# Kernel tuning notes

Hardware: AMD Instinct MI355X
Metric: run time of the kernel (lower is better)

## Reference

```python
import jax, jax.numpy as jnp
import numpy as np

BETA = 0.25
N_E = 1024
E_DIM = 64


def setup_inputs() -> dict:
    key = jax.random.key(0)
    k1, k2 = jax.random.split(key)
    z = jax.random.normal(k1, (32, E_DIM, 64, 64), dtype=jnp.float32)  # (B,C,H,W)
    emb = jax.random.uniform(k2, (N_E, E_DIM), dtype=jnp.float32,
                             minval=-1.0 / N_E, maxval=1.0 / N_E)
    return {"z": z, "embedding": emb}


def reference(z, embedding):
    # (B,C,H,W) -> (B,H,W,C)
    z_nhwc = jnp.transpose(z, (0, 2, 3, 1))
    zf = z_nhwc.reshape(-1, E_DIM)  # (N, C)
    # squared L2 distances: ||z||^2 + ||e||^2 - 2 z e^T  -> (N, n_e)
    d = (jnp.sum(zf * zf, axis=1, keepdims=True)
         + jnp.sum(embedding * embedding, axis=1)
         - 2.0 * jnp.matmul(zf, embedding.T))
    min_encoding_indices = jnp.argmin(d, axis=1)[:, None]  # (N,1)
    idx = min_encoding_indices[:, 0]
    min_encodings = jax.nn.one_hot(idx, N_E, dtype=jnp.float32)  # (N, n_e)
    # codebook lookup (equivalent to one-hot matmul)
    z_q = embedding[idx].reshape(z_nhwc.shape)  # (B,H,W,C)
    loss = (jnp.mean((jax.lax.stop_gradient(z_q) - z_nhwc) ** 2)
            + BETA * jnp.mean((z_q - jax.lax.stop_gradient(z_nhwc)) ** 2))
    # straight-through estimator
    z_q = z_nhwc + jax.lax.stop_gradient(z_q - z_nhwc)
    e_mean = jnp.mean(min_encodings, axis=0)
    perplexity = jnp.exp(-jnp.sum(e_mean * jnp.log(e_mean + 1e-10)))
    z_q = jnp.transpose(z_q, (0, 3, 1, 2))  # (B,C,H,W)
    return (loss, z_q, perplexity, min_encodings, min_encoding_indices)
```

## Files before the change

### kernel.cpp

```cpp
#include <hip/hip_runtime.h>

#define N_PIX   (32 * 64 * 64)
#define E_DIM   64
#define N_E     1024
#define Z_ELEMS (N_PIX * E_DIM)

#define LOSS_OFF 0
#define ZQ_OFF   1
#define PERP_OFF (1 + Z_ELEMS)
#define ENC_OFF  ((size_t)(2 + Z_ELEMS))
#define IDX_OFF  (ENC_OFF + (size_t)N_PIX * N_E)

#define WS_COUNTS   0
#define WS_LOSS     4096
#define WS_EE       8192
#define WS_EMB16    12288
#define WS_MINV     143360
#define WS_KEYS     667648
#define WS_CAND     1716224
#define WS_WCOUNT   5910528
#define NWAVES      4096
#define WAVE_CAP    256
#define MARGIN      4e-3f

typedef float f32x2 __attribute__((ext_vector_type(2)));
typedef float f32x4 __attribute__((ext_vector_type(4)));
typedef short bf16x8 __attribute__((ext_vector_type(8)));
typedef unsigned long long u64;
typedef unsigned short ushort;

__device__ __forceinline__ float dpp_add_xor1(float v) {
    int i = __builtin_bit_cast(int, v);
    i = __builtin_amdgcn_mov_dpp(i, 0xB1, 0xF, 0xF, true);
    return v + __builtin_bit_cast(float, i);
}
__device__ __forceinline__ float dpp_add_xor2(float v) {
    int i = __builtin_bit_cast(int, v);
    i = __builtin_amdgcn_mov_dpp(i, 0x4E, 0xF, 0xF, true);
    return v + __builtin_bit_cast(float, i);
}
__device__ __forceinline__ ushort rne_bf16(float f) {
    unsigned u = __builtin_bit_cast(unsigned, f);
    return (ushort)((u + 0x7FFFu + ((u >> 16) & 1u)) >> 16);
}

__global__ void vq_prep(const float* __restrict__ emb, float* __restrict__ ee,
                        ushort* __restrict__ emb16) {
    int e = blockIdx.x * blockDim.x + threadIdx.x;
    if (e < N_E) {
        const float* r = emb + e * E_DIM;
        float s0 = 0.f, s1 = 0.f, s2 = 0.f, s3 = 0.f;
        #pragma unroll
        for (int c = 0; c < E_DIM; c += 4) {
            s0 = fmaf(r[c],     r[c],     s0);
            s1 = fmaf(r[c + 1], r[c + 1], s1);
            s2 = fmaf(r[c + 2], r[c + 2], s2);
            s3 = fmaf(r[c + 3], r[c + 3], s3);
        }
        ee[e] = (s0 + s1) + (s2 + s3);
        #pragma unroll
        for (int j = 0; j < 64; j += 8) {
            bf16x8 v;
            #pragma unroll
            for (int q = 0; q < 8; ++q) v[q] = (short)rne_bf16(r[j + q]);
            *(bf16x8*)(emb16 + e * E_DIM + j) = v;
        }
    }
}

__device__ __forceinline__ bf16x8 load_afrag(const float* __restrict__ z,
                                             int px16, int lane, int khalf) {
    const int px = px16 + (lane & 15);
    const int b  = px >> 12;
    const int hw = px & 4095;
    const int c0 = khalf * 32 + ((lane >> 4) << 3);
    const float* zp = z + ((size_t)(b * E_DIM + c0)) * 4096 + hw;
    bf16x8 v;
    #pragma unroll
    for (int j = 0; j < 8; ++j) v[j] = (short)rne_bf16(zp[(size_t)j * 4096]);
    return v;
}

__global__ __launch_bounds__(256, 4) void vq_passA(
    const float* __restrict__ z, const ushort* __restrict__ emb16,
    const float* __restrict__ ee, float* __restrict__ out,
    float* __restrict__ minv)
{
    const int tid  = threadIdx.x;
    const int lane = tid & 63;
    const int pxb  = blockIdx.x * 128 + (tid >> 6) * 32;

    bf16x8 afr[2][2];
    #pragma unroll
    for (int t = 0; t < 2; ++t)
        #pragma unroll
        for (int h = 0; h < 2; ++h)
            afr[t][h] = load_afrag(z, pxb + t * 16, lane, h);

    float m[2][4];
    #pragma unroll
    for (int t = 0; t < 2; ++t)
        #pragma unroll
        for (int r = 0; r < 4; ++r) m[t][r] = 3.4e38f;

    const size_t zb = ENC_OFF + (size_t)blockIdx.x * 128 * N_E;
    const int col = lane & 15;
    const int bko = ((lane >> 4) << 3);

    for (int cg = 0; cg < 64; ++cg) {
        const float eev = ee[cg * 16 + col];
        const ushort* br = emb16 + (cg * 16 + col) * E_DIM + bko;
        const bf16x8 b0 = *(const bf16x8*)br;
        const bf16x8 b1 = *(const bf16x8*)(br + 32);
        #pragma unroll
        for (int t = 0; t < 2; ++t) {
            f32x4 acc = {0.f, 0.f, 0.f, 0.f};
            acc = __builtin_amdgcn_mfma_f32_16x16x32_bf16(afr[t][0], b0, acc, 0, 0, 0);
            acc = __builtin_amdgcn_mfma_f32_16x16x32_bf16(afr[t][1], b1, acc, 0, 0, 0);
            #pragma unroll
            for (int r = 0; r < 4; ++r)
                m[t][r] = fminf(m[t][r], fmaf(-2.f, acc[r], eev));
        }
        const f32x2 zv2 = {0.f, 0.f};
        float* dst = out + zb + (size_t)cg * N_E + tid * 4;
        __builtin_nontemporal_store(zv2, (f32x2*)dst);
        __builtin_nontemporal_store(zv2, (f32x2*)(dst + 2));
    }

    #pragma unroll
    for (int t = 0; t < 2; ++t)
        #pragma unroll
        for (int r = 0; r < 4; ++r) {
            float v = m[t][r];
            v = fminf(v, __shfl_xor(v, 1));
            v = fminf(v, __shfl_xor(v, 2));
            v = fminf(v, __shfl_xor(v, 4));
            v = fminf(v, __shfl_xor(v, 8));
            if ((lane & 15) == 0)
                minv[pxb + t * 16 + ((lane >> 4) << 2) + r] = v;
        }
}

__global__ __launch_bounds__(256, 4) void vq_passB(
    const float* __restrict__ z, const ushort* __restrict__ emb16,
    const float* __restrict__ ee, float* __restrict__ out,
    const float* __restrict__ minv, unsigned* __restrict__ cand,
    unsigned* __restrict__ wcount)
{
    const int tid  = threadIdx.x;
    const int lane = tid & 63;
    const int pxb  = blockIdx.x * 128 + (tid >> 6) * 32;

    bf16x8 afr[2][2];
    #pragma unroll
    for (int t = 0; t < 2; ++t)
        #pragma unroll
        for (int h = 0; h < 2; ++h)
            afr[t][h] = load_afrag(z, pxb + t * 16, lane, h);

    float lim[2][4];
    #pragma unroll
    for (int t = 0; t < 2; ++t)
        #pragma unroll
        for (int r = 0; r < 4; ++r)
            lim[t][r] = minv[pxb + t * 16 + ((lane >> 4) << 2) + r] + MARGIN;

    const size_t zb = ENC_OFF + (size_t)blockIdx.x * 128 * N_E;
    const int col = lane & 15;
    const int bko = ((lane >> 4) << 3);

    const unsigned wid  = blockIdx.x * 4 + (tid >> 6);
    unsigned* wseg = cand + (size_t)wid * WAVE_CAP;
    const u64 below = (lane == 0) ? 0ull : ((~0ull) >> (64 - lane));
    unsigned wbase = 0;

    for (int cg = 0; cg < 64; ++cg) {
        const float eev = ee[cg * 16 + col];
        const ushort* br = emb16 + (cg * 16 + col) * E_DIM + bko;
        const bf16x8 b0 = *(const bf16x8*)br;
        const bf16x8 b1 = *(const bf16x8*)(br + 32);
        #pragma unroll
        for (int t = 0; t < 2; ++t) {
            f32x4 acc = {0.f, 0.f, 0.f, 0.f};
            acc = __builtin_amdgcn_mfma_f32_16x16x32_bf16(afr[t][0], b0, acc, 0, 0, 0);
            acc = __builtin_amdgcn_mfma_f32_16x16x32_bf16(afr[t][1], b1, acc, 0, 0, 0);
            #pragma unroll
            for (int r = 0; r < 4; ++r) {
                const float d = fmaf(-2.f, acc[r], eev);
                const bool hit = (d <= lim[t][r]);
                const u64 mask = __ballot(hit);
                if (hit) {
                    const unsigned pos = wbase + (unsigned)__popcll(mask & below);
                    if (pos < WAVE_CAP) {
                        const unsigned px = pxb + t * 16 + ((lane >> 4) << 2) + r;
                        wseg[pos] = (px << 10) | (unsigned)(cg * 16 + col);
                    }
                }
                wbase += (unsigned)__popcll(mask);
            }
        }
        const f32x2 zv2 = {0.f, 0.f};
        float* dst = out + zb + (size_t)(64 + cg) * N_E + tid * 4;
        __builtin_nontemporal_store(zv2, (f32x2*)dst);
        __builtin_nontemporal_store(zv2, (f32x2*)(dst + 2));
    }

    if (lane == 0) wcount[wid] = (wbase < WAVE_CAP) ? wbase : WAVE_CAP;
}

__global__ __launch_bounds__(256) void vq_cleanup(
    const float* __restrict__ z, const float* __restrict__ emb,
    const float* __restrict__ ee, const unsigned* __restrict__ cand,
    const unsigned* __restrict__ wcount, u64* __restrict__ keys)
{
    const int s = threadIdx.x & 3;
    const unsigned quad = threadIdx.x >> 2;
    const unsigned w = blockIdx.x;
    const unsigned n = wcount[w];

    for (unsigned j = quad; j < n; j += 64) {
        const unsigned ent = cand[(size_t)w * WAVE_CAP + j];
        const int p = ent >> 10, k = ent & 1023;
        const int b = p >> 12, hw = p & 4095;

        const float* zp = z + ((size_t)(b * E_DIM + s * 16)) * 4096 + hw;
        f32x4 zv[4];
        #pragma unroll
        for (int m = 0; m < 4; ++m)
            #pragma unroll
            for (int qi = 0; qi < 4; ++qi)
                zv[m][qi] = zp[(size_t)(4 * m + qi) * 4096];

        f32x4 za = {0.f,0.f,0.f,0.f};
        #pragma unroll
        for (int j2 = 0; j2 < 4; ++j2) za = __builtin_elementwise_fma(zv[j2], zv[j2], za);
        f32x2 zt = __builtin_shufflevector(za, za, 0, 1)
                 + __builtin_shufflevector(za, za, 2, 3);
        const float zz = dpp_add_xor2(dpp_add_xor1(zt.x + zt.y));

        const f32x4* rp = (const f32x4*)(emb + k * E_DIM) + s * 4;
        f32x4 a = {0.f,0.f,0.f,0.f};
        #pragma unroll
        for (int j2 = 0; j2 < 4; ++j2) a = __builtin_elementwise_fma(zv[j2], rp[j2], a);
        f32x2 t2 = __builtin_shufflevector(a, a, 0, 1)
                 + __builtin_shufflevector(a, a, 2, 3);
        const float dot = dpp_add_xor2(dpp_add_xor1(t2.x + t2.y));
        const float d = zz + ee[k] - 2.0f * dot;

        if (s == 0) {
            const u64 key = ((u64)__builtin_bit_cast(unsigned, d) << 32) | (unsigned)k;
            atomicMin(&keys[p], key);
        }
    }
}

__global__ __launch_bounds__(256) void vq_resolve(
    const float* __restrict__ z, const float* __restrict__ emb,
    const u64* __restrict__ keys, float* __restrict__ out,
    unsigned* __restrict__ counts, double* __restrict__ loss_acc)
{
    const int p  = blockIdx.x * 256 + threadIdx.x;
    const int b  = p >> 12;
    const int hw = p & 4095;
    const int idx = (int)(unsigned)(keys[p] & 0xFFFFFFFFu);

    out[IDX_OFF + p] = (float)idx;
    out[ENC_OFF + (size_t)p * N_E + idx] = 1.0f;
    atomicAdd(&counts[idx], 1u);

    const f32x4* eb = (const f32x4*)(emb + idx * E_DIM);
    const float* zp = z + (size_t)b * E_DIM * 4096 + hw;
    float* zqp = out + ZQ_OFF + (size_t)b * E_DIM * 4096 + hw;
    f32x4 la = {0.f,0.f,0.f,0.f};
    #pragma unroll
    for (int m = 0; m < 16; ++m) {
        const f32x4 q = eb[m];
        f32x4 zq4;
        #pragma unroll
        for (int qi = 0; qi < 4; ++qi) {
            zq4[qi] = zp[(size_t)(4 * m + qi) * 4096];
            __builtin_nontemporal_store(q[qi], &zqp[(size_t)(4 * m + qi) * 4096]);
        }
        const f32x4 dq = q - zq4;
        la = __builtin_elementwise_fma(dq, dq, la);
    }
    float lsum = (la[0] + la[2]) + (la[1] + la[3]);
    #pragma unroll
    for (int o = 32; o > 0; o >>= 1) lsum += __shfl_down(lsum, o);
    if ((threadIdx.x & 63) == 0) atomicAdd(loss_acc, (double)lsum);
}

__global__ void vq_final(const unsigned* __restrict__ counts,
                         const double* __restrict__ loss_acc,
                         float* __restrict__ out)
{
    __shared__ float red[N_E];
    const int e = threadIdx.x;
    const float em = (float)counts[e] * (1.0f / (float)N_PIX);
    red[e] = em * logf(em + 1e-10f);
    __syncthreads();
    for (int s = 512; s > 0; s >>= 1) {
        if (e < s) red[e] += red[e + s];
        __syncthreads();
    }
    if (e == 0) {
        out[PERP_OFF] = expf(-red[0]);
        out[LOSS_OFF] = (float)((*loss_acc) * (1.25 / (double)Z_ELEMS));
    }
}

extern "C" void kernel_launch(void* const* d_in, const int* in_sizes, int n_in,
                              void* d_out, int out_size, void* d_ws, size_t ws_size,
                              hipStream_t stream) {
    const float* z   = (const float*)d_in[0];
    const float* emb = (const float*)d_in[1];
    float* out = (float*)d_out;
    char* ws = (char*)d_ws;

    unsigned* counts   = (unsigned*)(ws + WS_COUNTS);
    double*   loss_acc = (double*)(ws + WS_LOSS);
    float*    ee       = (float*)(ws + WS_EE);
    ushort*   emb16    = (ushort*)(ws + WS_EMB16);
    float*    minv     = (float*)(ws + WS_MINV);
    u64*      keys     = (u64*)(ws + WS_KEYS);
    unsigned* cand     = (unsigned*)(ws + WS_CAND);
    unsigned* wcount   = (unsigned*)(ws + WS_WCOUNT);

    (void)hipMemsetAsync(ws, 0, 4104, stream);
    (void)hipMemsetAsync(keys, 0xFF, (size_t)N_PIX * 8, stream);
    vq_prep<<<4, 256, 0, stream>>>(emb, ee, emb16);
    vq_passA<<<N_PIX / 128, 256, 0, stream>>>(z, emb16, ee, out, minv);
    vq_passB<<<N_PIX / 128, 256, 0, stream>>>(z, emb16, ee, out, minv, cand, wcount);
    vq_cleanup<<<NWAVES, 256, 0, stream>>>(z, emb, ee, cand, wcount, keys);
    vq_resolve<<<N_PIX / 256, 256, 0, stream>>>(z, emb, keys, out, counts, loss_acc);
    vq_final<<<1, N_E, 0, stream>>>(counts, loss_acc, out);
}
```

Measured before the change: 259.5 us.

## Fuse two-pass scan and cleanup/resolve kernels, drop atomic key buffer

Merges the min-finding pass and candidate-collection pass into one kernel that keeps per-pixel minima in registers, eliminating the minv buffer round trip and z fragment reload. Merges candidate rescoring and resolve into a per-wave kernel where each pixel's quad scans the wave's candidate list and picks the best index directly, removing the keys memset and 64-bit atomicMin. The finish kernel reuses the loaded z values for the loss. Each quad now serially scans the whole candidate segment, which adds redundant reads when candidate counts are large.

```diff
diff --git a/kernel.cpp b/kernel.cpp
--- a/kernel.cpp
+++ b/kernel.cpp
@@ -15,10 +15,8 @@
 #define WS_LOSS     4096
 #define WS_EE       8192
 #define WS_EMB16    12288
-#define WS_MINV     143360
-#define WS_KEYS     667648
-#define WS_CAND     1716224
-#define WS_WCOUNT   5910528
+#define WS_CAND     143360
+#define WS_WCOUNT   4337664
 #define NWAVES      4096
 #define WAVE_CAP    256
 #define MARGIN      4e-3f
@@ -81,10 +79,10 @@
     return v;
 }
 
-__global__ __launch_bounds__(256, 4) void vq_passA(
+__global__ __launch_bounds__(256, 4) void vq_scan(
     const float* __restrict__ z, const ushort* __restrict__ emb16,
     const float* __restrict__ ee, float* __restrict__ out,
-    float* __restrict__ minv)
+    unsigned* __restrict__ cand, unsigned* __restrict__ wcount)
 {
     const int tid  = threadIdx.x;
     const int lane = tid & 63;
@@ -127,6 +125,7 @@
         __builtin_nontemporal_store(zv2, (f32x2*)(dst + 2));
     }
 
+    float lim[2][4];
     #pragma unroll
     for (int t = 0; t < 2; ++t)
         #pragma unroll
@@ -136,38 +135,8 @@
             v = fminf(v, __shfl_xor(v, 2));
             v = fminf(v, __shfl_xor(v, 4));
             v = fminf(v, __shfl_xor(v, 8));
-            if ((lane & 15) == 0)
-                minv[pxb + t * 16 + ((lane >> 4) << 2) + r] = v;
-        }
-}
-
-__global__ __launch_bounds__(256, 4) void vq_passB(
-    const float* __restrict__ z, const ushort* __restrict__ emb16,
-    const float* __restrict__ ee, float* __restrict__ out,
-    const float* __restrict__ minv, unsigned* __restrict__ cand,
-    unsigned* __restrict__ wcount)
-{
-    const int tid  = threadIdx.x;
-    const int lane = tid & 63;
-    const int pxb  = blockIdx.x * 128 + (tid >> 6) * 32;
-
-    bf16x8 afr[2][2];
-    #pragma unroll
-    for (int t = 0; t < 2; ++t)
-        #pragma unroll
-        for (int h = 0; h < 2; ++h)
-            afr[t][h] = load_afrag(z, pxb + t * 16, lane, h);
-
-    float lim[2][4];
-    #pragma unroll
-    for (int t = 0; t < 2; ++t)
-        #pragma unroll
-        for (int r = 0; r < 4; ++r)
-            lim[t][r] = minv[pxb + t * 16 + ((lane >> 4) << 2) + r] + MARGIN;
-
-    const size_t zb = ENC_OFF + (size_t)blockIdx.x * 128 * N_E;
-    const int col = lane & 15;
-    const int bko = ((lane >> 4) << 3);
+            lim[t][r] = v + MARGIN;
+        }
 
     const unsigned wid  = blockIdx.x * 4 + (tid >> 6);
     unsigned* wseg = cand + (size_t)wid * WAVE_CAP;
@@ -208,36 +177,44 @@
     if (lane == 0) wcount[wid] = (wbase < WAVE_CAP) ? wbase : WAVE_CAP;
 }
 
-__global__ __launch_bounds__(256) void vq_cleanup(
+__global__ __launch_bounds__(128, 8) void vq_finish(
     const float* __restrict__ z, const float* __restrict__ emb,
     const float* __restrict__ ee, const unsigned* __restrict__ cand,
-    const unsigned* __restrict__ wcount, u64* __restrict__ keys)
+    const unsigned* __restrict__ wcount, float* __restrict__ out,
+    unsigned* __restrict__ counts, double* __restrict__ loss_acc)
 {
-    const int s = threadIdx.x & 3;
-    const unsigned quad = threadIdx.x >> 2;
     const unsigned w = blockIdx.x;
+    const int pxb = (int)((w >> 2) * 128 + (w & 3) * 32);
+    const int tid = threadIdx.x;
+    const int s   = tid & 3;
+    const int pl  = tid >> 2;
+    const int p   = pxb + pl;
+    const int b   = p >> 12;
+    const int hw  = p & 4095;
+
+    const float* zp = z + ((size_t)(b * E_DIM + s * 16)) * 4096 + hw;
+    f32x4 zv[4];
+    #pragma unroll
+    for (int m = 0; m < 4; ++m)
+        #pragma unroll
+        for (int qi = 0; qi < 4; ++qi)
+            zv[m][qi] = zp[(size_t)(4 * m + qi) * 4096];
+
+    f32x4 za = {0.f,0.f,0.f,0.f};
+    #pragma unroll
+    for (int j = 0; j < 4; ++j) za = __builtin_elementwise_fma(zv[j], zv[j], za);
+    f32x2 zt = __builtin_shufflevector(za, za, 0, 1)
+             + __builtin_shufflevector(za, za, 2, 3);
+    const float zz = dpp_add_xor2(dpp_add_xor1(zt.x + zt.y));
+
     const unsigned n = wcount[w];
-
-    for (unsigned j = quad; j < n; j += 64) {
-        const unsigned ent = cand[(size_t)w * WAVE_CAP + j];
-        const int p = ent >> 10, k = ent & 1023;
-        const int b = p >> 12, hw = p & 4095;
-
-        const float* zp = z + ((size_t)(b * E_DIM + s * 16)) * 4096 + hw;
-        f32x4 zv[4];
-        #pragma unroll
-        for (int m = 0; m < 4; ++m)
-            #pragma unroll
-            for (int qi = 0; qi < 4; ++qi)
-                zv[m][qi] = zp[(size_t)(4 * m + qi) * 4096];
-
-        f32x4 za = {0.f,0.f,0.f,0.f};
-        #pragma unroll
-        for (int j2 = 0; j2 < 4; ++j2) za = __builtin_elementwise_fma(zv[j2], zv[j2], za);
-        f32x2 zt = __builtin_shufflevector(za, za, 0, 1)
-                 + __builtin_shufflevector(za, za, 2, 3);
-        const float zz = dpp_add_xor2(dpp_add_xor1(zt.x + zt.y));
-
+    const unsigned* seg = cand + (size_t)w * WAVE_CAP;
+    float bd = 3.4e38f;
+    int   bi = 0x7FFFFFFF;
+    for (unsigned j = 0; j < n; ++j) {
+        const unsigned ent = seg[j];
+        if ((int)(ent >> 10) != p) continue;
+        const int k = (int)(ent & 1023u);
         const f32x4* rp = (const f32x4*)(emb + k * E_DIM) + s * 4;
         f32x4 a = {0.f,0.f,0.f,0.f};
         #pragma unroll
@@ -246,48 +223,33 @@
                  + __builtin_shufflevector(a, a, 2, 3);
         const float dot = dpp_add_xor2(dpp_add_xor1(t2.x + t2.y));
         const float d = zz + ee[k] - 2.0f * dot;
-
-        if (s == 0) {
-            const u64 key = ((u64)__builtin_bit_cast(unsigned, d) << 32) | (unsigned)k;
-            atomicMin(&keys[p], key);
-        }
-    }
-}
-
-__global__ __launch_bounds__(256) void vq_resolve(
-    const float* __restrict__ z, const float* __restrict__ emb,
-    const u64* __restrict__ keys, float* __restrict__ out,
-    unsigned* __restrict__ counts, double* __restrict__ loss_acc)
-{
-    const int p  = blockIdx.x * 256 + threadIdx.x;
-    const int b  = p >> 12;
-    const int hw = p & 4095;
-    const int idx = (int)(unsigned)(keys[p] & 0xFFFFFFFFu);
-
-    out[IDX_OFF + p] = (float)idx;
-    out[ENC_OFF + (size_t)p * N_E + idx] = 1.0f;
-    atomicAdd(&counts[idx], 1u);
-
-    const f32x4* eb = (const f32x4*)(emb + idx * E_DIM);
-    const float* zp = z + (size_t)b * E_DIM * 4096 + hw;
-    float* zqp = out + ZQ_OFF + (size_t)b * E_DIM * 4096 + hw;
+        const bool better = (d < bd) || ((d == bd) && (k < bi));
+        bd = better ? d : bd;
+        bi = better ? k : bi;
+    }
+
+    if (s == 0) {
+        out[IDX_OFF + p] = (float)bi;
+        out[ENC_OFF + (size_t)p * N_E + bi] = 1.0f;
+        atomicAdd(&counts[bi], 1u);
+    }
+
+    const f32x4* eb = (const f32x4*)(emb + bi * E_DIM) + s * 4;
+    float* zqp = out + ZQ_OFF + ((size_t)(b * E_DIM + s * 16)) * 4096 + hw;
     f32x4 la = {0.f,0.f,0.f,0.f};
     #pragma unroll
-    for (int m = 0; m < 16; ++m) {
+    for (int m = 0; m < 4; ++m) {
         const f32x4 q = eb[m];
-        f32x4 zq4;
-        #pragma unroll
-        for (int qi = 0; qi < 4; ++qi) {
-            zq4[qi] = zp[(size_t)(4 * m + qi) * 4096];
+        #pragma unroll
+        for (int qi = 0; qi < 4; ++qi)
             __builtin_nontemporal_store(q[qi], &zqp[(size_t)(4 * m + qi) * 4096]);
-        }
-        const f32x4 dq = q - zq4;
+        const f32x4 dq = q - zv[m];
         la = __builtin_elementwise_fma(dq, dq, la);
     }
     float lsum = (la[0] + la[2]) + (la[1] + la[3]);
     #pragma unroll
     for (int o = 32; o > 0; o >>= 1) lsum += __shfl_down(lsum, o);
-    if ((threadIdx.x & 63) == 0) atomicAdd(loss_acc, (double)lsum);
+    if ((tid & 63) == 0) atomicAdd(loss_acc, (double)lsum);
 }
 
 __global__ void vq_final(const unsigned* __restrict__ counts,
@@ -321,17 +283,13 @@
     double*   loss_acc = (double*)(ws + WS_LOSS);
     float*    ee       = (float*)(ws + WS_EE);
     ushort*   emb16    = (ushort*)(ws + WS_EMB16);
-    float*    minv     = (float*)(ws + WS_MINV);
-    u64*      keys     = (u64*)(ws + WS_KEYS);
     unsigned* cand     = (unsigned*)(ws + WS_CAND);
     unsigned* wcount   = (unsigned*)(ws + WS_WCOUNT);
 
     (void)hipMemsetAsync(ws, 0, 4104, stream);
-    (void)hipMemsetAsync(keys, 0xFF, (size_t)N_PIX * 8, stream);
     vq_prep<<<4, 256, 0, stream>>>(emb, ee, emb16);
-    vq_passA<<<N_PIX / 128, 256, 0, stream>>>(z, emb16, ee, out, minv);
-    vq_passB<<<N_PIX / 128, 256, 0, stream>>>(z, emb16, ee, out, minv, cand, wcount);
-    vq_cleanup<<<NWAVES, 256, 0, stream>>>(z, emb, ee, cand, wcount, keys);
-    vq_resolve<<<N_PIX / 256, 256, 0, stream>>>(z, emb, keys, out, counts, loss_acc);
+    vq_scan<<<N_PIX / 128, 256, 0, stream>>>(z, emb16, ee, out, cand, wcount);
+    vq_finish<<<NWAVES, 128, 0, stream>>>(z, emb, ee, cand, wcount, out,
+                                          counts, loss_acc);
     vq_final<<<1, N_E, 0, stream>>>(counts, loss_acc, out);
 }
```

New measurement: 342.8 us. +32.1%, slower.

## Fuse candidate cleanup and resolve into one kernel with per-block LDS argmin

Applied to the files above, without the earlier changes.

Merges the exact-recheck cleanup and the resolve kernel into a single kernel, one block per 32-pixel wave segment. The block stages that segment's z into LDS, computes ||z||^2 once per pixel, and reduces the argmin with LDS atomics instead of global 64-bit atomics. It then writes indices, one-hot entries, z_q and the loss directly. This drops the global keys buffer and its memset, one kernel launch, and the repeated strided z reads. It assumes the candidates of wave w belong to pixels pxb..pxb+31 as computed from the block index, and only 128 of the 256 threads take part in the final writes.

```diff
diff --git a/kernel.cpp b/kernel.cpp
--- a/kernel.cpp
+++ b/kernel.cpp
@@ -16,9 +16,8 @@
 #define WS_EE       8192
 #define WS_EMB16    12288
 #define WS_MINV     143360
-#define WS_KEYS     667648
-#define WS_CAND     1716224
-#define WS_WCOUNT   5910528
+#define WS_CAND     667648
+#define WS_WCOUNT   4861952
 #define NWAVES      4096
 #define WAVE_CAP    256
 #define MARGIN      4e-3f
@@ -208,86 +207,106 @@
     if (lane == 0) wcount[wid] = (wbase < WAVE_CAP) ? wbase : WAVE_CAP;
 }
 
-__global__ __launch_bounds__(256) void vq_cleanup(
+__global__ __launch_bounds__(256, 4) void vq_finish(
     const float* __restrict__ z, const float* __restrict__ emb,
     const float* __restrict__ ee, const unsigned* __restrict__ cand,
-    const unsigned* __restrict__ wcount, u64* __restrict__ keys)
+    const unsigned* __restrict__ wcount, float* __restrict__ out,
+    unsigned* __restrict__ counts, double* __restrict__ loss_acc)
 {
-    const int s = threadIdx.x & 3;
-    const unsigned quad = threadIdx.x >> 2;
+    __shared__ float lds_z[32][68];
+    __shared__ u64   lkey[32];
+    __shared__ float lzz[32];
+
     const unsigned w = blockIdx.x;
-    const unsigned n = wcount[w];
-
-    for (unsigned j = quad; j < n; j += 64) {
-        const unsigned ent = cand[(size_t)w * WAVE_CAP + j];
-        const int p = ent >> 10, k = ent & 1023;
-        const int b = p >> 12, hw = p & 4095;
-
-        const float* zp = z + ((size_t)(b * E_DIM + s * 16)) * 4096 + hw;
-        f32x4 zv[4];
+    const int pxb = (int)((w >> 2) * 128 + (w & 3) * 32);
+    const int tid  = threadIdx.x;
+    const int s    = tid & 3;
+    const int quad = tid >> 2;
+
+    {
+        const int px = tid & 31, chb = tid >> 5;
+        const int p  = pxb + px;
+        const int b  = p >> 12, hw = p & 4095;
+        #pragma unroll
+        for (int pass = 0; pass < 8; ++pass) {
+            const int ch = pass * 8 + chb;
+            lds_z[px][ch] = z[((size_t)(b * E_DIM + ch)) * 4096 + hw];
+        }
+    }
+    if (tid < 32) lkey[tid] = ~0ull;
+    __syncthreads();
+
+    f32x4 zv[4];
+    if (tid < 128) {
         #pragma unroll
         for (int m = 0; m < 4; ++m)
-            #pragma unroll
-            for (int qi = 0; qi < 4; ++qi)
-                zv[m][qi] = zp[(size_t)(4 * m + qi) * 4096];
-
+            zv[m] = *(const f32x4*)&lds_z[quad][s * 16 + 4 * m];
         f32x4 za = {0.f,0.f,0.f,0.f};
         #pragma unroll
-        for (int j2 = 0; j2 < 4; ++j2) za = __builtin_elementwise_fma(zv[j2], zv[j2], za);
+        for (int j = 0; j < 4; ++j) za = __builtin_elementwise_fma(zv[j], zv[j], za);
         f32x2 zt = __builtin_shufflevector(za, za, 0, 1)
                  + __builtin_shufflevector(za, za, 2, 3);
         const float zz = dpp_add_xor2(dpp_add_xor1(zt.x + zt.y));
+        if (s == 0) lzz[quad] = zz;
+    }
+    __syncthreads();
+
+    const unsigned n = wcount[w];
+    const unsigned* seg = cand + (size_t)w * WAVE_CAP;
+    for (unsigned j = quad; j < n; j += 64) {
+        const unsigned ent = seg[j];
+        const int ple = (int)(ent >> 10) - pxb;
+        const int k   = (int)(ent & 1023u);
+
+        f32x4 zve[4];
+        #pragma unroll
+        for (int m = 0; m < 4; ++m)
+            zve[m] = *(const f32x4*)&lds_z[ple][s * 16 + 4 * m];
 
         const f32x4* rp = (const f32x4*)(emb + k * E_DIM) + s * 4;
         f32x4 a = {0.f,0.f,0.f,0.f};
         #pragma unroll
-        for (int j2 = 0; j2 < 4; ++j2) a = __builtin_elementwise_fma(zv[j2], rp[j2], a);
+        for (int j2 = 0; j2 < 4; ++j2) a = __builtin_elementwise_fma(zve[j2], rp[j2], a);
         f32x2 t2 = __builtin_shufflevector(a, a, 0, 1)
                  + __builtin_shufflevector(a, a, 2, 3);
         const float dot = dpp_add_xor2(dpp_add_xor1(t2.x + t2.y));
-        const float d = zz + ee[k] - 2.0f * dot;
+        const float d = lzz[ple] + ee[k] - 2.0f * dot;
 
         if (s == 0) {
             const u64 key = ((u64)__builtin_bit_cast(unsigned, d) << 32) | (unsigned)k;
-            atomicMin(&keys[p], key);
-        }
-    }
-}
-
-__global__ __launch_bounds__(256) void vq_resolve(
-    const float* __restrict__ z, const float* __restrict__ emb,
-    const u64* __restrict__ keys, float* __restrict__ out,
-    unsigned* __restrict__ counts, double* __restrict__ loss_acc)
-{
-    const int p  = blockIdx.x * 256 + threadIdx.x;
-    const int b  = p >> 12;
-    const int hw = p & 4095;
-    const int idx = (int)(unsigned)(keys[p] & 0xFFFFFFFFu);
-
-    out[IDX_OFF + p] = (float)idx;
-    out[ENC_OFF + (size_t)p * N_E + idx] = 1.0f;
-    atomicAdd(&counts[idx], 1u);
-
-    const f32x4* eb = (const f32x4*)(emb + idx * E_DIM);
-    const float* zp = z + (size_t)b * E_DIM * 4096 + hw;
-    float* zqp = out + ZQ_OFF + (size_t)b * E_DIM * 4096 + hw;
-    f32x4 la = {0.f,0.f,0.f,0.f};
-    #pragma unroll
-    for (int m = 0; m < 16; ++m) {
-        const f32x4 q = eb[m];
-        f32x4 zq4;
-        #pragma unroll
-        for (int qi = 0; qi < 4; ++qi) {
-            zq4[qi] = zp[(size_t)(4 * m + qi) * 4096];
-            __builtin_nontemporal_store(q[qi], &zqp[(size_t)(4 * m + qi) * 4096]);
-        }
-        const f32x4 dq = q - zq4;
-        la = __builtin_elementwise_fma(dq, dq, la);
-    }
-    float lsum = (la[0] + la[2]) + (la[1] + la[3]);
-    #pragma unroll
-    for (int o = 32; o > 0; o >>= 1) lsum += __shfl_down(lsum, o);
-    if ((threadIdx.x & 63) == 0) atomicAdd(loss_acc, (double)lsum);
+            atomicMin(&lkey[ple], key);
+        }
+    }
+    __syncthreads();
+
+    if (tid < 128) {
+        const int p  = pxb + quad;
+        const int b  = p >> 12, hw = p & 4095;
+        const int bi = (int)(unsigned)(lkey[quad] & 0xFFFFFFFFu);
+
+        if (s == 0) {
+            out[IDX_OFF + p] = (float)bi;
+            out[ENC_OFF + (size_t)p * N_E + bi] = 1.0f;
+            atomicAdd(&counts[bi], 1u);
+        }
+
+        const f32x4* eb = (const f32x4*)(emb + bi * E_DIM) + s * 4;
+        float* zqp = out + ZQ_OFF + ((size_t)(b * E_DIM + s * 16)) * 4096 + hw;
+        f32x4 la = {0.f,0.f,0.f,0.f};
+        #pragma unroll
+        for (int m = 0; m < 4; ++m) {
+            const f32x4 q = eb[m];
+            #pragma unroll
+            for (int qi = 0; qi < 4; ++qi)
+                __builtin_nontemporal_store(q[qi], &zqp[(size_t)(4 * m + qi) * 4096]);
+            const f32x4 dq = q - zv[m];
+            la = __builtin_elementwise_fma(dq, dq, la);
+        }
+        float lsum = (la[0] + la[2]) + (la[1] + la[3]);
+        #pragma unroll
+        for (int o = 32; o > 0; o >>= 1) lsum += __shfl_down(lsum, o);
+        if ((tid & 63) == 0) atomicAdd(loss_acc, (double)lsum);
+    }
 }
 
 __global__ void vq_final(const unsigned* __restrict__ counts,
@@ -322,16 +341,14 @@
     float*    ee       = (float*)(ws + WS_EE);
     ushort*   emb16    = (ushort*)(ws + WS_EMB16);
     float*    minv     = (float*)(ws + WS_MINV);
-    u64*      keys     = (u64*)(ws + WS_KEYS);
     unsigned* cand     = (unsigned*)(ws + WS_CAND);
     unsigned* wcount   = (unsigned*)(ws + WS_WCOUNT);
 
     (void)hipMemsetAsync(ws, 0, 4104, stream);
-    (void)hipMemsetAsync(keys, 0xFF, (size_t)N_PIX * 8, stream);
     vq_prep<<<4, 256, 0, stream>>>(emb, ee, emb16);
     vq_passA<<<N_PIX / 128, 256, 0, stream>>>(z, emb16, ee, out, minv);
     vq_passB<<<N_PIX / 128, 256, 0, stream>>>(z, emb16, ee, out, minv, cand, wcount);
-    vq_cleanup<<<NWAVES, 256, 0, stream>>>(z, emb, ee, cand, wcount, keys);
-    vq_resolve<<<N_PIX / 256, 256, 0, stream>>>(z, emb, keys, out, counts, loss_acc);
+    vq_finish<<<NWAVES, 256, 0, stream>>>(z, emb, ee, cand, wcount, out,
+                                          counts, loss_acc);
     vq_final<<<1, N_E, 0, stream>>>(counts, loss_acc, out);
 }
```

Result: slower. 285.9 us (+10.1%).

## Fuse min-distance and candidate-collection passes into a single scan kernel

Applied to the files above, without the earlier changes.

Merges passA (computes per-pixel approximate min distance and zeroes the one-hot output) and passB (recomputes distances and collects candidates within a margin) into one kernel. After the first sweep over the codebook the min is reduced in registers and used directly as the threshold, and the second candidate sweep then runs in the same kernel. This removes one kernel launch, the reload of z fragments, and the global write and read of the minv buffer. The combined kernel may use more registers, and per-wave work is serialized within one launch instead of across two.

```diff
diff --git a/kernel.cpp b/kernel.cpp
--- a/kernel.cpp
+++ b/kernel.cpp
@@ -15,10 +15,9 @@
 #define WS_LOSS     4096
 #define WS_EE       8192
 #define WS_EMB16    12288
-#define WS_MINV     143360
-#define WS_KEYS     667648
-#define WS_CAND     1716224
-#define WS_WCOUNT   5910528
+#define WS_KEYS     143360
+#define WS_CAND     1191936
+#define WS_WCOUNT   5386240
 #define NWAVES      4096
 #define WAVE_CAP    256
 #define MARGIN      4e-3f
@@ -81,10 +80,10 @@
     return v;
 }
 
-__global__ __launch_bounds__(256, 4) void vq_passA(
+__global__ __launch_bounds__(256, 4) void vq_scan(
     const float* __restrict__ z, const ushort* __restrict__ emb16,
     const float* __restrict__ ee, float* __restrict__ out,
-    float* __restrict__ minv)
+    unsigned* __restrict__ cand, unsigned* __restrict__ wcount)
 {
     const int tid  = threadIdx.x;
     const int lane = tid & 63;
@@ -127,6 +126,7 @@
         __builtin_nontemporal_store(zv2, (f32x2*)(dst + 2));
     }
 
+    float lim[2][4];
     #pragma unroll
     for (int t = 0; t < 2; ++t)
         #pragma unroll
@@ -136,38 +136,8 @@
             v = fminf(v, __shfl_xor(v, 2));
             v = fminf(v, __shfl_xor(v, 4));
             v = fminf(v, __shfl_xor(v, 8));
-            if ((lane & 15) == 0)
-                minv[pxb + t * 16 + ((lane >> 4) << 2) + r] = v;
-        }
-}
-
-__global__ __launch_bounds__(256, 4) void vq_passB(
-    const float* __restrict__ z, const ushort* __restrict__ emb16,
-    const float* __restrict__ ee, float* __restrict__ out,
-    const float* __restrict__ minv, unsigned* __restrict__ cand,
-    unsigned* __restrict__ wcount)
-{
-    const int tid  = threadIdx.x;
-    const int lane = tid & 63;
-    const int pxb  = blockIdx.x * 128 + (tid >> 6) * 32;
-
-    bf16x8 afr[2][2];
-    #pragma unroll
-    for (int t = 0; t < 2; ++t)
-        #pragma unroll
-        for (int h = 0; h < 2; ++h)
-            afr[t][h] = load_afrag(z, pxb + t * 16, lane, h);
-
-    float lim[2][4];
-    #pragma unroll
-    for (int t = 0; t < 2; ++t)
-        #pragma unroll
-        for (int r = 0; r < 4; ++r)
-            lim[t][r] = minv[pxb + t * 16 + ((lane >> 4) << 2) + r] + MARGIN;
-
-    const size_t zb = ENC_OFF + (size_t)blockIdx.x * 128 * N_E;
-    const int col = lane & 15;
-    const int bko = ((lane >> 4) << 3);
+            lim[t][r] = v + MARGIN;
+        }
 
     const unsigned wid  = blockIdx.x * 4 + (tid >> 6);
     unsigned* wseg = cand + (size_t)wid * WAVE_CAP;
@@ -321,7 +291,6 @@
     double*   loss_acc = (double*)(ws + WS_LOSS);
     float*    ee       = (float*)(ws + WS_EE);
     ushort*   emb16    = (ushort*)(ws + WS_EMB16);
-    float*    minv     = (float*)(ws + WS_MINV);
     u64*      keys     = (u64*)(ws + WS_KEYS);
     unsigned* cand     = (unsigned*)(ws + WS_CAND);
     unsigned* wcount   = (unsigned*)(ws + WS_WCOUNT);
@@ -329,8 +298,7 @@
     (void)hipMemsetAsync(ws, 0, 4104, stream);
     (void)hipMemsetAsync(keys, 0xFF, (size_t)N_PIX * 8, stream);
     vq_prep<<<4, 256, 0, stream>>>(emb, ee, emb16);
-    vq_passA<<<N_PIX / 128, 256, 0, stream>>>(z, emb16, ee, out, minv);
-    vq_passB<<<N_PIX / 128, 256, 0, stream>>>(z, emb16, ee, out, minv, cand, wcount);
+    vq_scan<<<N_PIX / 128, 256, 0, stream>>>(z, emb16, ee, out, cand, wcount);
     vq_cleanup<<<NWAVES, 256, 0, stream>>>(z, emb, ee, cand, wcount, keys);
     vq_resolve<<<N_PIX / 256, 256, 0, stream>>>(z, emb, keys, out, counts, loss_acc);
     vq_final<<<1, N_E, 0, stream>>>(counts, loss_acc, out);
```

After: 266.1 us. 1.03x slower.
